# Optimization experiments

Measured on AMD Instinct MI355X. Metric: run time of the kernel, lower is better.

The kernel has to match this reference:

```python
import jax, jax.numpy as jnp
import numpy as np

B, N, F = 4096, 16384, 16384
MEAN_SUB = 0.1  # fraction of mean activity subtracted (from original: mean_activity * 0.1)


def setup_inputs() -> dict:
    key = jax.random.key(0)
    k1, k2, k3 = jax.random.split(key, 3)
    encoded_features = jax.random.normal(k1, (B, F), dtype=jnp.float32)
    # original init: rand*0.4 + 0.8 scaled by a sin-based competition factor; rand in [0.8,1.2) is faithful enough
    specialization_weights = jax.random.uniform(k2, (N,), dtype=jnp.float32) * 0.4 + 0.8
    feature_preferences = jax.random.randint(k3, (N,), 0, F, dtype=jnp.int32)
    return {
        "encoded_features": encoded_features,
        "specialization_weights": specialization_weights,
        "feature_preferences": feature_preferences,
    }


def reference(encoded_features, specialization_weights, feature_preferences):
    # per-neuron gather of its preferred feature (pref % F), scaled by specialization weight
    pref = jnp.mod(feature_preferences, encoded_features.shape[-1])
    gathered = jnp.take(encoded_features, pref, axis=-1)          # [B, N]
    specialized = gathered * specialization_weights[None, :]       # [B, N]
    # competitive normalization: subtract 0.1 * mean activity, then half-wave rectify
    mean_activity = jnp.mean(specialized, axis=-1, keepdims=True)  # [B, 1]
    return jnp.maximum(specialized - MEAN_SUB * mean_activity, 0.0)
```

## Files before the change

kernel.cpp:

```cpp
#include <hip/hip_runtime.h>


constexpr int B_ROWS  = 4096;
constexpr int N_NEUR  = 16384;
constexpr int F_FEAT  = 16384;
constexpr int THREADS = 512;
constexpr int VPT     = N_NEUR / THREADS;
constexpr int CHUNK   = 4;
constexpr int ITERS   = VPT / CHUNK;
constexpr float MEAN_SUB = 0.1f;

__global__ void __launch_bounds__(THREADS, 4)
sensory_kernel(const float* __restrict__ enc,
               const float* __restrict__ w,
               const int*   __restrict__ pref,
               float*       __restrict__ out) {
    __shared__ float row[F_FEAT];

    const int tid = threadIdx.x;
    const int b   = blockIdx.x;

    const float4* __restrict__ rowg4 = (const float4*)(enc + (size_t)b * F_FEAT);
    float4* row4 = (float4*)row;
    #pragma unroll
    for (int j = 0; j < F_FEAT / 4 / THREADS; ++j) {
        row4[tid + j * THREADS] = rowg4[tid + j * THREADS];
    }
    __syncthreads();

    float v[VPT];
    float lsum = 0.0f;
    #pragma unroll
    for (int k = 0; k < ITERS; ++k) {
        const int n = k * (THREADS * CHUNK) + tid * CHUNK;
        const int4   p4 = *(const int4*)(pref + n);
        const float4 w4 = *(const float4*)(w + n);
        const float a0 = row[p4.x & (F_FEAT - 1)] * w4.x;
        const float a1 = row[p4.y & (F_FEAT - 1)] * w4.y;
        const float a2 = row[p4.z & (F_FEAT - 1)] * w4.z;
        const float a3 = row[p4.w & (F_FEAT - 1)] * w4.w;
        v[k * 4 + 0] = a0;
        v[k * 4 + 1] = a1;
        v[k * 4 + 2] = a2;
        v[k * 4 + 3] = a3;
        lsum += (a0 + a1) + (a2 + a3);
    }

    #pragma unroll
    for (int off = 32; off > 0; off >>= 1)
        lsum += __shfl_down(lsum, off, 64);

    __syncthreads();
    if ((tid & 63) == 0) row[tid >> 6] = lsum;
    __syncthreads();
    if (tid == 0) {
        float t = 0.0f;
        #pragma unroll
        for (int i = 0; i < THREADS / 64; ++i) t += row[i];
        row[0] = t * (MEAN_SUB / (float)N_NEUR);
    }
    __syncthreads();
    const float sub = row[0];

    float* __restrict__ outrow = out + (size_t)b * N_NEUR;
    #pragma unroll
    for (int k = 0; k < ITERS; ++k) {
        const int n = k * (THREADS * CHUNK) + tid * CHUNK;
        float4 o;
        o.x = fmaxf(v[k * 4 + 0] - sub, 0.0f);
        o.y = fmaxf(v[k * 4 + 1] - sub, 0.0f);
        o.z = fmaxf(v[k * 4 + 2] - sub, 0.0f);
        o.w = fmaxf(v[k * 4 + 3] - sub, 0.0f);
        *(float4*)(outrow + n) = o;
    }
}

extern "C" void kernel_launch(void* const* d_in, const int* in_sizes, int n_in,
                              void* d_out, int out_size, void* d_ws, size_t ws_size,
                              hipStream_t stream) {
    const float* enc  = (const float*)d_in[0];
    const float* w    = (const float*)d_in[1];
    const int*   pref = (const int*)d_in[2];
    float*       out  = (float*)d_out;
    sensory_kernel<<<B_ROWS, THREADS, 0, stream>>>(enc, w, pref, out);
}
```

Before: 434.6 us.

## Compute row mean via precomputed per-feature weight histogram dot product

Adds a small pre-kernel that scatters the specialization weights into a per-feature coefficient vector c. The row mean then becomes a dot product of the row with c, computed while the row is staged into shared memory. This removes the gather pass that held 32 values per thread in registers before the reduction. The gather is redone in the output pass instead. Block size also grows to 1024 threads. The costs are an extra launch, a single-block atomic pre-pass, reading c once per row, and a different floating-point summation order.

```diff
diff --git a/kernel.cpp b/kernel.cpp
--- a/kernel.cpp
+++ b/kernel.cpp
@@ -4,16 +4,37 @@
 constexpr int B_ROWS  = 4096;
 constexpr int N_NEUR  = 16384;
 constexpr int F_FEAT  = 16384;
-constexpr int THREADS = 512;
-constexpr int VPT     = N_NEUR / THREADS;
-constexpr int CHUNK   = 4;
-constexpr int ITERS   = VPT / CHUNK;
 constexpr float MEAN_SUB = 0.1f;
 
-__global__ void __launch_bounds__(THREADS, 4)
+constexpr int T_MAIN = 1024;
+constexpr int ITER4  = F_FEAT / 4 / T_MAIN;
+
+__global__ void __launch_bounds__(1024)
+build_c_kernel(const float* __restrict__ w, const int* __restrict__ pref,
+               float* __restrict__ c_out) {
+    __shared__ float c[F_FEAT];
+    const int tid = threadIdx.x;
+    float4* c4 = (float4*)c;
+    #pragma unroll
+    for (int j = 0; j < F_FEAT / 4 / 1024; ++j)
+        c4[tid + j * 1024] = make_float4(0.f, 0.f, 0.f, 0.f);
+    __syncthreads();
+    #pragma unroll
+    for (int j = 0; j < N_NEUR / 1024; ++j) {
+        const int n = tid + j * 1024;
+        atomicAdd(&c[pref[n] & (F_FEAT - 1)], w[n]);
+    }
+    __syncthreads();
+    #pragma unroll
+    for (int j = 0; j < F_FEAT / 4 / 1024; ++j)
+        ((float4*)c_out)[tid + j * 1024] = c4[tid + j * 1024];
+}
+
+__global__ void __launch_bounds__(T_MAIN, 8)
 sensory_kernel(const float* __restrict__ enc,
                const float* __restrict__ w,
                const int*   __restrict__ pref,
+               const float* __restrict__ c,
                float*       __restrict__ out) {
     __shared__ float row[F_FEAT];
 
@@ -21,57 +42,46 @@
     const int b   = blockIdx.x;
 
     const float4* __restrict__ rowg4 = (const float4*)(enc + (size_t)b * F_FEAT);
+    const float4* __restrict__ cg4   = (const float4*)c;
     float4* row4 = (float4*)row;
+    float dot = 0.f;
     #pragma unroll
-    for (int j = 0; j < F_FEAT / 4 / THREADS; ++j) {
-        row4[tid + j * THREADS] = rowg4[tid + j * THREADS];
+    for (int j = 0; j < ITER4; ++j) {
+        const int i = tid + j * T_MAIN;
+        const float4 e  = rowg4[i];
+        const float4 cc = cg4[i];
+        row4[i] = e;
+        dot += (e.x * cc.x + e.y * cc.y) + (e.z * cc.z + e.w * cc.w);
     }
-    __syncthreads();
-
-    float v[VPT];
-    float lsum = 0.0f;
-    #pragma unroll
-    for (int k = 0; k < ITERS; ++k) {
-        const int n = k * (THREADS * CHUNK) + tid * CHUNK;
-        const int4   p4 = *(const int4*)(pref + n);
-        const float4 w4 = *(const float4*)(w + n);
-        const float a0 = row[p4.x & (F_FEAT - 1)] * w4.x;
-        const float a1 = row[p4.y & (F_FEAT - 1)] * w4.y;
-        const float a2 = row[p4.z & (F_FEAT - 1)] * w4.z;
-        const float a3 = row[p4.w & (F_FEAT - 1)] * w4.w;
-        v[k * 4 + 0] = a0;
-        v[k * 4 + 1] = a1;
-        v[k * 4 + 2] = a2;
-        v[k * 4 + 3] = a3;
-        lsum += (a0 + a1) + (a2 + a3);
-    }
-
     #pragma unroll
     for (int off = 32; off > 0; off >>= 1)
-        lsum += __shfl_down(lsum, off, 64);
+        dot += __shfl_down(dot, off, 64);
 
     __syncthreads();
-    if ((tid & 63) == 0) row[tid >> 6] = lsum;
+    float save = (tid < T_MAIN / 64) ? row[tid] : 0.f;
     __syncthreads();
-    if (tid == 0) {
-        float t = 0.0f;
-        #pragma unroll
-        for (int i = 0; i < THREADS / 64; ++i) t += row[i];
-        row[0] = t * (MEAN_SUB / (float)N_NEUR);
-    }
+    if ((tid & 63) == 0) row[tid >> 6] = dot;
     __syncthreads();
-    const float sub = row[0];
+    float tot = 0.f;
+    #pragma unroll
+    for (int i = 0; i < T_MAIN / 64; ++i) tot += row[i];
+    const float sub = tot * (MEAN_SUB / (float)N_NEUR);
+    __syncthreads();
+    if (tid < T_MAIN / 64) row[tid] = save;
+    __syncthreads();
 
     float* __restrict__ outrow = out + (size_t)b * N_NEUR;
     #pragma unroll
-    for (int k = 0; k < ITERS; ++k) {
-        const int n = k * (THREADS * CHUNK) + tid * CHUNK;
+    for (int k = 0; k < ITER4; ++k) {
+        const int i  = tid + k * T_MAIN;
+        const int4   p4 = ((const int4*)pref)[i];
+        const float4 w4 = ((const float4*)w)[i];
         float4 o;
-        o.x = fmaxf(v[k * 4 + 0] - sub, 0.0f);
-        o.y = fmaxf(v[k * 4 + 1] - sub, 0.0f);
-        o.z = fmaxf(v[k * 4 + 2] - sub, 0.0f);
-        o.w = fmaxf(v[k * 4 + 3] - sub, 0.0f);
-        *(float4*)(outrow + n) = o;
+        o.x = fmaxf(row[p4.x & (F_FEAT - 1)] * w4.x - sub, 0.f);
+        o.y = fmaxf(row[p4.y & (F_FEAT - 1)] * w4.y - sub, 0.f);
+        o.z = fmaxf(row[p4.z & (F_FEAT - 1)] * w4.z - sub, 0.f);
+        o.w = fmaxf(row[p4.w & (F_FEAT - 1)] * w4.w - sub, 0.f);
+        ((float4*)outrow)[i] = o;
     }
 }
 
@@ -82,5 +92,8 @@
     const float* w    = (const float*)d_in[1];
     const int*   pref = (const int*)d_in[2];
     float*       out  = (float*)d_out;
-    sensory_kernel<<<B_ROWS, THREADS, 0, stream>>>(enc, w, pref, out);
+    float*       c    = (float*)d_ws;
+
+    build_c_kernel<<<1, 1024, 0, stream>>>(w, pref, c);
+    sensory_kernel<<<B_ROWS, T_MAIN, 0, stream>>>(enc, w, pref, c, out);
 }
```

New measurement: 458.9 us. 1.06x slower.
